# Kernel optimization log

Hardware: AMD Instinct MI355X
Metric: run time of the kernel (lower is better)

## Reference

```python
import jax, jax.numpy as jnp
import numpy as np

B, N, K, H = 8, 1024, 16, 4
EMB = 1024

def lrelu(x):
    return jnp.where(x >= 0, x, 0.2 * x)

def bn(x, g, b):
    # eval-mode BatchNorm with running_mean=0, running_var=1
    inv = 1.0 / np.sqrt(1.0 + 1e-5)
    shape = (1, -1) + (1,) * (x.ndim - 2)
    return x * (g * inv).reshape(shape) + b.reshape(shape)

def conv1x1(x, w):
    # 1x1 conv == channel matmul; x: (B,C,...), w: (O,C)
    return jnp.einsum('bc...,oc->bo...', x, w)

def knn_idx(x, k):
    # x: (B,C,N); negative squared pairwise distance, top-k largest = nearest
    inner = -2.0 * jnp.einsum('bcn,bcm->bnm', x, x)
    xx = jnp.sum(x * x, axis=1)                      # (B,N)
    pd = -xx[:, :, None] - inner - xx[:, None, :]
    return jax.lax.top_k(pd, k)[1]                   # (B,N,k)

def graph_feature(x, idx):
    b = x.shape[0]
    xt = jnp.transpose(x, (0, 2, 1))                 # (B,N,C)
    nbr = xt[jnp.arange(b)[:, None, None], idx]      # (B,N,K,C) gather
    ctr = jnp.broadcast_to(xt[:, :, None, :], nbr.shape)
    f = jnp.concatenate([nbr - ctr, ctr], axis=-1)   # (B,N,K,2C)
    return jnp.transpose(f, (0, 3, 1, 2))            # (B,2C,N,K)

def mak(x, y, w0, g0, b0, wm, gm, bm, w1, go, bo, ws, gs, bs, out_ch, in_ch):
    # Multi-head adaptive kernel: generate per-point (out,in,H) weights from y, apply to x
    Bc, _, Nc, Kc = x.shape
    y = lrelu(bn(conv1x1(y, w0), g0, b0))
    y = lrelu(bn(conv1x1(y, wm), gm, bm))
    y = conv1x1(y, w1)                               # (B, out*in*H, N, K)
    w = jnp.transpose(y, (0, 2, 3, 1)).reshape(Bc, Nc, Kc, out_ch, in_ch, H)
    xt = jnp.transpose(x, (0, 2, 3, 1))              # (B,N,K,in)
    # per-head matmul then sum over heads == single einsum over i and h
    out = jnp.einsum('bnkoih,bnki->bonk', w, xt)
    out = bn(out, go, bo)
    idt = bn(conv1x1(x, ws), gs, bs)                 # shortcut (in != out)
    return lrelu(out + idt)


def setup_inputs() -> dict:
    ks = jax.random.split(jax.random.key(0), 48)
    it = iter(range(48))
    def nrm(shape, fan):
        return jax.random.normal(ks[next(it)], shape, jnp.float32) / np.sqrt(fan)
    def gam(c):
        return jax.random.uniform(ks[next(it)], (c,), jnp.float32, 0.5, 1.5)
    def bet(c):
        return 0.1 * jax.random.normal(ks[next(it)], (c,), jnp.float32)
    d = {}
    d['x'] = jax.random.normal(ks[next(it)], (B, 3, N), jnp.float32)
    def mak_params(p, feat_c):
        d[p + '_w0'] = nrm((64, feat_c), feat_c); d[p + '_g0'] = gam(64); d[p + '_b0'] = bet(64)
        d[p + '_wm'] = nrm((64, 64), 64); d[p + '_gm'] = gam(64); d[p + '_bm'] = bet(64)
        d[p + '_w1'] = nrm((64 * 6 * H, 64), 64)
        d[p + '_go'] = gam(64); d[p + '_bo'] = bet(64)
        d[p + '_ws'] = nrm((64, 6), 6); d[p + '_gs'] = gam(64); d[p + '_bs'] = bet(64)
    mak_params('m1', 6)
    mak_params('m2', 128)
    d['w3'] = nrm((128, 128), 128); d['g3'] = gam(128); d['b3'] = bet(128)
    d['w4'] = nrm((256, 256), 256); d['g4'] = gam(256); d['b4'] = bet(256)
    d['w5'] = nrm((EMB, 512), 512); d['g5'] = gam(EMB); d['b5'] = bet(EMB)
    d['wl1'] = nrm((512, 2 * EMB), 2 * EMB); d['bn4_g'] = gam(512); d['bn4_b'] = bet(512)
    d['wl2'] = nrm((256, 512), 512); d['bl2'] = bet(256); d['bn5_g'] = gam(256); d['bn5_b'] = bet(256)
    d['wl3'] = nrm((49, 256), 256); d['bl3'] = bet(49)
    return d


def reference(x, m1_w0, m1_g0, m1_b0, m1_wm, m1_gm, m1_bm, m1_w1, m1_go, m1_bo, m1_ws, m1_gs, m1_bs, m2_w0, m2_g0, m2_b0, m2_wm, m2_gm, m2_bm, m2_w1, m2_go, m2_bo, m2_ws, m2_gs, m2_bs, w3, g3, b3, w4, g4, b4, w5, g5, b5, wl1, bn4_g, bn4_b, wl2, bl2, bn5_g, bn5_b, wl3, bl3):
    idx = knn_idx(x, K)                              # common_idx from points
    geo = graph_feature(x, idx)                      # (B,6,N,K); feat_x == geo_x at stage 1
    h = mak(geo, geo, m1_w0, m1_g0, m1_b0, m1_wm, m1_gm, m1_bm, m1_w1, m1_go, m1_bo, m1_ws, m1_gs, m1_bs, 64, 6)
    x1 = h.max(axis=-1)                              # (B,64,N)
    feat2 = graph_feature(x1, idx)                   # (B,128,N,K)
    h = mak(geo, feat2, m2_w0, m2_g0, m2_b0, m2_wm, m2_gm, m2_bm, m2_w1, m2_go, m2_bo, m2_ws, m2_gs, m2_bs, 64, 6)
    x2 = h.max(axis=-1)                              # (B,64,N)
    x3 = lrelu(bn(conv1x1(graph_feature(x2, idx), w3), g3, b3)).max(axis=-1)   # (B,128,N)
    x4 = lrelu(bn(conv1x1(graph_feature(x3, idx), w4), g4, b4)).max(axis=-1)   # (B,256,N)
    xc = jnp.concatenate([x1, x2, x3, x4], axis=1)   # (B,512,N)
    x5 = lrelu(bn(conv1x1(xc, w5), g5, b5))          # (B,EMB,N)
    xp = jnp.concatenate([x5.max(axis=-1), x5.mean(axis=-1)], axis=1)  # (B,2*EMB)
    xf = lrelu(bn(xp @ wl1.T, bn4_g, bn4_b))
    xf = lrelu(bn(xf @ wl2.T + bl2, bn5_g, bn5_b))
    return xf @ wl3.T + bl3                           # (B,49)
```

## Files before the change

### kernel.cpp

```cpp
#include <hip/hip_runtime.h>
#include <math.h>

#define BB 8
#define NN 1024
#define KK 16
#define NKP (NN*KK)
#define BN_INV 0.99999500003749981f

typedef unsigned short u16;
typedef __attribute__((ext_vector_type(8))) short short8;
typedef __attribute__((ext_vector_type(4))) float f32x4;

#define MFMA16(a,b,c) __builtin_amdgcn_mfma_f32_16x16x32_bf16(a,b,c,0,0,0)

__device__ __forceinline__ float lrelu(float v) { return v >= 0.f ? v : 0.2f * v; }

__device__ __forceinline__ u16 f2bf(float f) {
  union { float f; unsigned u; } v; v.f = f;
  unsigned r = v.u + 0x7fff + ((v.u >> 16) & 1);
  return (u16)(r >> 16);
}
__device__ __forceinline__ float bf2f(u16 s) {
  union { unsigned u; float f; } v; v.u = ((unsigned)s) << 16;
  return v.f;
}

constexpr size_t OFF_IDX   = 0;
constexpr size_t OFF_X1P   = 524288;
constexpr size_t OFF_X2P   = 1572864;
constexpr size_t OFF_X3P   = 2621440;
constexpr size_t OFF_X4P   = 4718592;
constexpr size_t OFF_PMAX  = 8912896;
constexpr size_t OFF_PSUM  = 9437184;
constexpr size_t OFF_XP    = 9961472;
constexpr size_t OFF_XF1   = 10027008;
constexpr size_t OFF_XF2   = 10043392;
constexpr size_t OFF_M1W0  = 10051584;
constexpr size_t OFF_M1WM  = 10055680;
constexpr size_t OFF_M1W1S = 10063872;
constexpr size_t OFF_M2W0  = 10117120;
constexpr size_t OFF_M2WM  = 10133504;
constexpr size_t OFF_M2W1S = 10141696;
constexpr size_t OFF_W3    = 10194944;
constexpr size_t OFF_W4    = 10227712;
constexpr size_t OFF_W5    = 10358784;
constexpr size_t OFF_WL1T  = 11407360;
constexpr size_t OFF_WL2T  = 15601664;
constexpr size_t OFF_WL3T  = 16125952;

struct SSeg { const float* w; const float* g; u16* dst; int O; int C; int cpl2; int ch; int start; };
struct SArgs { SSeg seg[7]; int total; };

__global__ __launch_bounds__(256) void prep_scale_bf16(SArgs a) {
  const int tid = blockIdx.x * 256 + threadIdx.x;
  if (tid >= a.total) return;
  int s = 0;
  #pragma unroll
  for (int i = 1; i < 7; ++i) if (tid >= a.seg[i].start) s = i;
  const SSeg sg = a.seg[s];
  const int e = tid - sg.start;
  const int o = e >> sg.cpl2;
  const int c = e & ((1 << sg.cpl2) - 1);
  float v = 0.f;
  if (c < sg.C) {
    v = sg.w[o * sg.C + c];
    if (sg.ch && c >= sg.ch) v -= sg.w[o * sg.C + c - sg.ch];
    v *= sg.g[o] * BN_INV;
  }
  sg.dst[(size_t)(c >> 5) * (sg.O * 32) + o * 32 + (c & 31)] = f2bf(v);
}

__global__ __launch_bounds__(256) void prep_w1s_bf16(
    const float* __restrict__ w1a, const float* __restrict__ wsa,
    const float* __restrict__ goa, const float* __restrict__ gsa,
    const float* __restrict__ w1b, const float* __restrict__ wsb,
    const float* __restrict__ gob, const float* __restrict__ gsb,
    u16* __restrict__ dsta, u16* __restrict__ dstb) {
  const int tid = blockIdx.x * 256 + threadIdx.x;
  if (tid >= 64 * 416) return;
  const float* w1 = blockIdx.y ? w1b : w1a;
  const float* wsm = blockIdx.y ? wsb : wsa;
  const float* go = blockIdx.y ? gob : goa;
  const float* gs = blockIdx.y ? gsb : gsa;
  u16* dst = blockIdx.y ? dstb : dsta;
  const int o = tid / 416, ci = tid - o * 416;
  float v = 0.f;
  if (ci < 384) {
    const int ii = ci >> 6, ch = ci & 63;
    const int base = (o * 24 + ii * 4) * 64 + ch;
    v = go[o] * BN_INV * (w1[base] + w1[base + 64] + w1[base + 128] + w1[base + 192]);
  } else if (ci < 390) {
    v = gs[o] * BN_INV * wsm[o * 6 + (ci - 384)];
  }
  dst[(size_t)(ci >> 5) * 2048 + o * 32 + (ci & 31)] = f2bf(v);
}

struct TSeg { const float* w; const float* g; float* dst; int O; int C; int start; };
struct TArgs3 { TSeg seg[3]; int total; };

__global__ __launch_bounds__(256) void prep_transpose_f32(TArgs3 a) {
  const int tid = blockIdx.x * 256 + threadIdx.x;
  if (tid >= a.total) return;
  int s = 0;
  #pragma unroll
  for (int i = 1; i < 3; ++i) if (tid >= a.seg[i].start) s = i;
  const TSeg sg = a.seg[s];
  const int e = tid - sg.start;
  const int c = e / sg.O;
  const int o = e - c * sg.O;
  float v = sg.w[o * sg.C + c];
  if (sg.g) v *= sg.g[o] * BN_INV;
  sg.dst[e] = v;
}

__global__ __launch_bounds__(256) void knn_kernel(const float* __restrict__ x, int* __restrict__ idxout) {
  const int wid  = (blockIdx.x * blockDim.x + threadIdx.x) >> 6;
  const int lane = threadIdx.x & 63;
  const int b = wid >> 10;
  const int n = wid & (NN - 1);
  const float* xb = x + b * 3 * NN;
  const float x0n = xb[n], x1n = xb[NN + n], x2n = xb[2 * NN + n];
  const float xxn = x0n * x0n + x1n * x1n + x2n * x2n;
  float pd[16];
  #pragma unroll
  for (int j = 0; j < 16; ++j) {
    const int m = j * 64 + lane;
    const float x0 = xb[m], x1 = xb[NN + m], x2 = xb[2 * NN + m];
    const float dot = x0n * x0 + x1n * x1 + x2n * x2;
    const float xxm = x0 * x0 + x1 * x1 + x2 * x2;
    pd[j] = 2.f * dot - xxn - xxm;
  }
  for (int r = 0; r < 16; ++r) {
    float bv = pd[0]; int bj = 0;
    #pragma unroll
    for (int j = 1; j < 16; ++j) if (pd[j] > bv) { bv = pd[j]; bj = j; }
    int bm = bj * 64 + lane;
    #pragma unroll
    for (int off = 32; off > 0; off >>= 1) {
      const float ov = __shfl_down(bv, off);
      const int   om = __shfl_down(bm, off);
      if (ov > bv || (ov == bv && om < bm)) { bv = ov; bm = om; }
    }
    bm = __shfl(bm, 0);
    if (lane == 0) idxout[wid * KK + r] = bm;
    const int  cj   = bm >> 6;
    const bool mine = (bm & 63) == lane;
    #pragma unroll
    for (int j = 0; j < 16; ++j) if (mine && j == cj) pd[j] = -INFINITY;
  }
}

__device__ __forceinline__ short8 bfrag64(const u16* T, int pl, int quad, int c0) {
  const int pos = ((c0 >> 3) + quad) ^ (pl & 7);
  return *(const short8*)(T + pl * 64 + pos * 8);
}
__device__ __forceinline__ void writeD64(u16* T, int pl, int quad, const f32x4 a,
                                         const float* __restrict__ bias, int obase) {
  union { ushort4 v; u16 s[4]; } pk;
  #pragma unroll
  for (int r = 0; r < 4; ++r) pk.s[r] = f2bf(lrelu(a[r] + bias[obase + quad * 4 + r]));
  const int g = (obase + quad * 4) >> 3;
  const int pos = g ^ (pl & 7);
  *(ushort4*)(T + pl * 64 + pos * 8 + (quad & 1) * 4) = pk.v;
}

template<int CIN_Y>
__global__ __launch_bounds__(256) void mak_mfma(
    const float* __restrict__ x, const int* __restrict__ idxb, const u16* __restrict__ srcp,
    const u16* __restrict__ w0b, const float* __restrict__ b0v,
    const u16* __restrict__ wmb, const float* __restrict__ bmv,
    const u16* __restrict__ w1s, const float* __restrict__ bov, const float* __restrict__ bsv,
    u16* __restrict__ Xoutp) {
  __shared__ __align__(16) u16 Y0s[64 * 64];
  __shared__ __align__(16) u16 YMs[64 * 64];
  __shared__ int nbrs[64];

  const int t = threadIdx.x;
  const int b = blockIdx.z;
  const int p0 = blockIdx.x * 64;
  const int w = t >> 6, l = t & 63;
  const int quad = l >> 4, l15 = l & 15;
  const int pl = w * 16 + l15;
  const int cq8 = quad * 8;
  const int nvtx = blockIdx.x * 4 + w;

  if (t < 64) nbrs[t] = idxb[b * NKP + p0 + t] & (NN - 1);
  __syncthreads();
  const int nbr = nbrs[pl];

  const float* xb = x + b * 3 * NN;
  float ge[6];
  #pragma unroll
  for (int i = 0; i < 3; ++i) {
    const float fc = xb[i * NN + nvtx];
    ge[i]     = xb[i * NN + nbr] - fc;
    ge[3 + i] = fc;
  }
  union { short8 v; u16 s[8]; } bg;
  bg.v = (short8)(short)0;
  if (quad == 0) {
    #pragma unroll
    for (int j = 0; j < 6; ++j) bg.s[j] = f2bf(ge[j]);
  }

  f32x4 acc[4];
  #pragma unroll
  for (int i = 0; i < 4; ++i) acc[i] = (f32x4)0.f;

  if constexpr (CIN_Y == 6) {
    #pragma unroll
    for (int at = 0; at < 4; ++at) {
      const short8 af = *(const short8*)(w0b + (size_t)(at * 16 + l15) * 32 + cq8);
      acc[at] = MFMA16(af, bg.v, acc[at]);
    }
  } else {
    short8 bf[4];
    #pragma unroll
    for (int k = 0; k < 2; ++k)
      bf[k] = *(const short8*)(srcp + (size_t)(b * NN + nbr) * 64 + k * 32 + cq8);
    #pragma unroll
    for (int k = 2; k < 4; ++k)
      bf[k] = *(const short8*)(srcp + (size_t)(b * NN + nvtx) * 64 + (k - 2) * 32 + cq8);
    #pragma unroll
    for (int k = 0; k < 4; ++k) {
      #pragma unroll
      for (int at = 0; at < 4; ++at) {
        const short8 af = *(const short8*)(w0b + (size_t)(k * 64 + at * 16 + l15) * 32 + cq8);
        acc[at] = MFMA16(af, bf[k], acc[at]);
      }
    }
  }
  #pragma unroll
  for (int at = 0; at < 4; ++at) writeD64(Y0s, pl, quad, acc[at], b0v, at * 16);
  __syncthreads();

  #pragma unroll
  for (int i = 0; i < 4; ++i) acc[i] = (f32x4)0.f;
  #pragma unroll
  for (int kc = 0; kc < 2; ++kc) {
    const short8 bf = bfrag64(Y0s, pl, quad, kc * 32);
    #pragma unroll
    for (int at = 0; at < 4; ++at) {
      const short8 af = *(const short8*)(wmb + (size_t)(kc * 64 + at * 16 + l15) * 32 + cq8);
      acc[at] = MFMA16(af, bf, acc[at]);
    }
  }
  #pragma unroll
  for (int at = 0; at < 4; ++at) writeD64(YMs, pl, quad, acc[at], bmv, at * 16);
  __syncthreads();

  #pragma unroll
  for (int i = 0; i < 4; ++i) acc[i] = (f32x4)0.f;
  #pragma unroll
  for (int ii = 0; ii < 6; ++ii) {
    f32x4 tacc[4];
    #pragma unroll
    for (int i = 0; i < 4; ++i) tacc[i] = (f32x4)0.f;
    #pragma unroll
    for (int kc = 0; kc < 2; ++kc) {
      const short8 bf = bfrag64(YMs, pl, quad, kc * 32);
      #pragma unroll
      for (int at = 0; at < 4; ++at) {
        const short8 af = *(const short8*)(w1s + (size_t)((ii * 2 + kc) * 64 + at * 16 + l15) * 32 + cq8);
        tacc[at] = MFMA16(af, bf, tacc[at]);
      }
    }
    const float g = ge[ii];
    #pragma unroll
    for (int at = 0; at < 4; ++at) acc[at] += g * tacc[at];
  }
  #pragma unroll
  for (int at = 0; at < 4; ++at) {
    const short8 af = *(const short8*)(w1s + (size_t)(12 * 64 + at * 16 + l15) * 32 + cq8);
    acc[at] = MFMA16(af, bg.v, acc[at]);
  }

  u16* orow = Xoutp + (size_t)(b * NN + nvtx) * 64;
  #pragma unroll
  for (int at = 0; at < 4; ++at) {
    union { ushort4 v; u16 s[4]; } pk;
    #pragma unroll
    for (int r = 0; r < 4; ++r) {
      const int o = at * 16 + quad * 4 + r;
      float v = lrelu(acc[at][r] + bov[o] + bsv[o]);
      v = fmaxf(v, __shfl_xor(v, 1));
      v = fmaxf(v, __shfl_xor(v, 2));
      v = fmaxf(v, __shfl_xor(v, 4));
      v = fmaxf(v, __shfl_xor(v, 8));
      pk.s[r] = f2bf(v);
    }
    if (l15 == 0) *(ushort4*)(orow + at * 16 + quad * 4) = pk.v;
  }
}

template<int CIN, int COUT>
__global__ __launch_bounds__(256) void conv_maxk_mfma(
    const u16* __restrict__ srcp, const int* __restrict__ idxb,
    const u16* __restrict__ wb, const float* __restrict__ bias,
    u16* __restrict__ Xoutp) {
  __shared__ int nbrs[64];
  constexpr int CH = CIN / 2;
  constexpr int NCH = CIN / 32;
  constexpr int NHB = CH / 32;
  constexpr int OPW = COUT / 4;
  constexpr int NAT = OPW / 16;

  const int t = threadIdx.x;
  const int b = blockIdx.z;
  const int p0 = blockIdx.x * 64;
  const int w = t >> 6, l = t & 63;
  const int quad = l >> 4, l15 = l & 15;
  const int cq8 = quad * 8;
  const int ow0 = w * OPW;

  if (t < 64) nbrs[t] = idxb[b * NKP + p0 + t] & (NN - 1);
  __syncthreads();

  int nbr[4], ctr[4];
  #pragma unroll
  for (int pg = 0; pg < 4; ++pg) {
    nbr[pg] = nbrs[pg * 16 + l15];
    ctr[pg] = blockIdx.x * 4 + pg;
  }

  f32x4 acc[NAT][4];
  #pragma unroll
  for (int i = 0; i < NAT; ++i)
    #pragma unroll
    for (int j = 0; j < 4; ++j) acc[i][j] = (f32x4)0.f;

  short8 bfr[NCH][4];
  #pragma unroll
  for (int k = 0; k < NHB; ++k) {
    const int c = k * 32 + cq8;
    #pragma unroll
    for (int pg = 0; pg < 4; ++pg)
      bfr[k][pg] = *(const short8*)(srcp + ((size_t)(b * NN + nbr[pg]) * CH + c));
  }
  #pragma unroll
  for (int k = NHB; k < NCH; ++k) {
    const int c = (k - NHB) * 32 + cq8;
    #pragma unroll
    for (int pg = 0; pg < 4; ++pg)
      bfr[k][pg] = *(const short8*)(srcp + ((size_t)(b * NN + ctr[pg]) * CH + c));
  }

  #pragma unroll
  for (int k = 0; k < NCH; ++k) {
    #pragma unroll
    for (int at = 0; at < NAT; ++at) {
      const short8 af = *(const short8*)(wb + ((size_t)(k * COUT + ow0 + at * 16 + l15)) * 32 + cq8);
      #pragma unroll
      for (int pg = 0; pg < 4; ++pg) acc[at][pg] = MFMA16(af, bfr[k][pg], acc[at][pg]);
    }
  }

  #pragma unroll
  for (int pg = 0; pg < 4; ++pg) {
    u16* orow = Xoutp + (size_t)(b * NN + ctr[pg]) * COUT + ow0;
    #pragma unroll
    for (int at = 0; at < NAT; ++at) {
      union { ushort4 v; u16 s[4]; } pk;
      #pragma unroll
      for (int r = 0; r < 4; ++r) {
        float v = lrelu(acc[at][pg][r] + bias[ow0 + at * 16 + quad * 4 + r]);
        v = fmaxf(v, __shfl_xor(v, 1));
        v = fmaxf(v, __shfl_xor(v, 2));
        v = fmaxf(v, __shfl_xor(v, 4));
        v = fmaxf(v, __shfl_xor(v, 8));
        pk.s[r] = f2bf(v);
      }
      if (l15 == 0) *(ushort4*)(orow + at * 16 + quad * 4) = pk.v;
    }
  }
}

__global__ __launch_bounds__(256) void conv5_mfma(
    const u16* __restrict__ X1P, const u16* __restrict__ X2P,
    const u16* __restrict__ X3P, const u16* __restrict__ X4P,
    const u16* __restrict__ w5b, const float* __restrict__ b5,
    float* __restrict__ PMAX, float* __restrict__ PSUM) {
  const int t = threadIdx.x;
  const int b = blockIdx.z;
  const int n0 = blockIdx.x * 64;
  const int w = t >> 6, l = t & 63;
  const int quad = l >> 4, l15 = l & 15;
  const int cq8 = quad * 8;
  const int ow0 = blockIdx.y * 256 + w * 64;

  f32x4 acc[4][4];
  #pragma unroll
  for (int i = 0; i < 4; ++i)
    #pragma unroll
    for (int j = 0; j < 4; ++j) acc[i][j] = (f32x4)0.f;

  #pragma unroll 4
  for (int k = 0; k < 16; ++k) {
    const int c = k * 32 + cq8;
    short8 bfr[4];
    #pragma unroll
    for (int pg = 0; pg < 4; ++pg) {
      const int n = n0 + pg * 16 + l15;
      const u16* src; int cc;
      if (c < 64)       { src = X1P + (size_t)(b * NN + n) * 64;  cc = c; }
      else if (c < 128) { src = X2P + (size_t)(b * NN + n) * 64;  cc = c - 64; }
      else if (c < 256) { src = X3P + (size_t)(b * NN + n) * 128; cc = c - 128; }
      else              { src = X4P + (size_t)(b * NN + n) * 256; cc = c - 256; }
      bfr[pg] = *(const short8*)(src + cc);
    }
    #pragma unroll
    for (int at = 0; at < 4; ++at) {
      const short8 af = *(const short8*)(w5b + ((size_t)(k * 1024 + ow0 + at * 16 + l15)) * 32 + cq8);
      #pragma unroll
      for (int pg = 0; pg < 4; ++pg) acc[at][pg] = MFMA16(af, bfr[pg], acc[at][pg]);
    }
  }

  #pragma unroll
  for (int at = 0; at < 4; ++at) {
    f32x4 pmx, psm;
    #pragma unroll
    for (int r = 0; r < 4; ++r) {
      const float bb = b5[ow0 + at * 16 + quad * 4 + r];
      float m = -INFINITY, s = 0.f;
      #pragma unroll
      for (int pg = 0; pg < 4; ++pg) {
        const float v = lrelu(acc[at][pg][r] + bb);
        m = fmaxf(m, v); s += v;
      }
      #pragma unroll
      for (int msk = 1; msk < 16; msk <<= 1) {
        m = fmaxf(m, __shfl_xor(m, msk));
        s += __shfl_xor(s, msk);
      }
      pmx[r] = m; psm[r] = s;
    }
    if (l15 == 0) {
      float* dm = PMAX + (size_t)(b * 16 + blockIdx.x) * 1024 + ow0 + at * 16 + quad * 4;
      float* ds = PSUM + (size_t)(b * 16 + blockIdx.x) * 1024 + ow0 + at * 16 + quad * 4;
      *(f32x4*)dm = pmx;
      *(f32x4*)ds = psm;
    }
  }
}

__global__ __launch_bounds__(256) void reduce5(const float* __restrict__ PMAX, const float* __restrict__ PSUM,
                                               float* __restrict__ XPg) {
  const int tid = blockIdx.x * 256 + threadIdx.x;
  const int b = tid >> 10, o = tid & 1023;
  float m = -INFINITY, s = 0.f;
  for (int pt = 0; pt < 16; ++pt) {
    m = fmaxf(m, PMAX[(size_t)(b * 16 + pt) * 1024 + o]);
    s += PSUM[(size_t)(b * 16 + pt) * 1024 + o];
  }
  XPg[b * 2048 + o] = m;
  XPg[b * 2048 + 1024 + o] = s * (1.f / 1024.f);
}

__global__ __launch_bounds__(256) void fc1_kernel(const float* __restrict__ XPg, const float* __restrict__ wl1t,
                                                  const float* __restrict__ bn4_b, float* __restrict__ XF1) {
  __shared__ float red[64 * 5];
  const int t = threadIdx.x;
  const int b = blockIdx.y;
  const int o = blockIdx.x * 64 + (t & 63);
  const int cq = t >> 6;
  const float* xp = XPg + b * 2048;
  float acc = 0.f;
  for (int c = cq * 512; c < cq * 512 + 512; ++c) acc = fmaf(wl1t[c * 512 + o], xp[c], acc);
  red[(t & 63) * 5 + cq] = acc;
  __syncthreads();
  if (t < 64) {
    const int oo = blockIdx.x * 64 + t;
    const float v = red[t * 5] + red[t * 5 + 1] + red[t * 5 + 2] + red[t * 5 + 3] + bn4_b[oo];
    XF1[b * 512 + oo] = lrelu(v);
  }
}

__global__ __launch_bounds__(256) void fc2_kernel(const float* __restrict__ XF1, const float* __restrict__ wl2t,
                                                  const float* __restrict__ bl2, const float* __restrict__ bn5_g,
                                                  const float* __restrict__ bn5_b, float* __restrict__ XF2) {
  __shared__ float red[64 * 5];
  const int t = threadIdx.x;
  const int b = blockIdx.y;
  const int o = blockIdx.x * 64 + (t & 63);
  const int cq = t >> 6;
  const float* xf = XF1 + b * 512;
  float acc = 0.f;
  for (int c = cq * 128; c < cq * 128 + 128; ++c) acc = fmaf(wl2t[c * 256 + o], xf[c], acc);
  red[(t & 63) * 5 + cq] = acc;
  __syncthreads();
  if (t < 64) {
    const int oo = blockIdx.x * 64 + t;
    const float bias = bl2[oo] * (bn5_g[oo] * BN_INV) + bn5_b[oo];
    const float v = red[t * 5] + red[t * 5 + 1] + red[t * 5 + 2] + red[t * 5 + 3] + bias;
    XF2[b * 256 + oo] = lrelu(v);
  }
}

__global__ __launch_bounds__(256) void fc3_kernel(const float* __restrict__ XF2, const float* __restrict__ wl3t,
                                                  const float* __restrict__ bl3, float* __restrict__ out) {
  __shared__ float red[64 * 5];
  const int t = threadIdx.x;
  const int b = blockIdx.y;
  const int ol = t & 63;
  const int cq = t >> 6;
  const float* xf = XF2 + b * 256;
  float acc = 0.f;
  if (ol < 49) for (int c = cq * 64; c < cq * 64 + 64; ++c) acc = fmaf(wl3t[c * 49 + ol], xf[c], acc);
  red[ol * 5 + cq] = acc;
  __syncthreads();
  if (t < 49) out[b * 49 + t] = red[t * 5] + red[t * 5 + 1] + red[t * 5 + 2] + red[t * 5 + 3] + bl3[t];
}

extern "C" void kernel_launch(void* const* d_in, const int* in_sizes, int n_in,
                              void* d_out, int out_size, void* d_ws, size_t ws_size,
                              hipStream_t stream) {
  (void)in_sizes; (void)n_in; (void)out_size; (void)ws_size;
  const float* x     = (const float*)d_in[0];
  const float* m1_w0 = (const float*)d_in[1];
  const float* m1_g0 = (const float*)d_in[2];
  const float* m1_b0 = (const float*)d_in[3];
  const float* m1_wm = (const float*)d_in[4];
  const float* m1_gm = (const float*)d_in[5];
  const float* m1_bm = (const float*)d_in[6];
  const float* m1_w1 = (const float*)d_in[7];
  const float* m1_go = (const float*)d_in[8];
  const float* m1_bo = (const float*)d_in[9];
  const float* m1_ws = (const float*)d_in[10];
  const float* m1_gs = (const float*)d_in[11];
  const float* m1_bs = (const float*)d_in[12];
  const float* m2_w0 = (const float*)d_in[13];
  const float* m2_g0 = (const float*)d_in[14];
  const float* m2_b0 = (const float*)d_in[15];
  const float* m2_wm = (const float*)d_in[16];
  const float* m2_gm = (const float*)d_in[17];
  const float* m2_bm = (const float*)d_in[18];
  const float* m2_w1 = (const float*)d_in[19];
  const float* m2_go = (const float*)d_in[20];
  const float* m2_bo = (const float*)d_in[21];
  const float* m2_ws = (const float*)d_in[22];
  const float* m2_gs = (const float*)d_in[23];
  const float* m2_bs = (const float*)d_in[24];
  const float* w3    = (const float*)d_in[25];
  const float* g3    = (const float*)d_in[26];
  const float* b3    = (const float*)d_in[27];
  const float* w4    = (const float*)d_in[28];
  const float* g4    = (const float*)d_in[29];
  const float* b4    = (const float*)d_in[30];
  const float* w5    = (const float*)d_in[31];
  const float* g5    = (const float*)d_in[32];
  const float* b5    = (const float*)d_in[33];
  const float* wl1   = (const float*)d_in[34];
  const float* bn4_g = (const float*)d_in[35];
  const float* bn4_b = (const float*)d_in[36];
  const float* wl2   = (const float*)d_in[37];
  const float* bl2   = (const float*)d_in[38];
  const float* bn5_g = (const float*)d_in[39];
  const float* bn5_b = (const float*)d_in[40];
  const float* wl3   = (const float*)d_in[41];
  const float* bl3   = (const float*)d_in[42];

  char* wsb = (char*)d_ws;
  int*  IDX  = (int*)(wsb + OFF_IDX);
  u16*  X1P  = (u16*)(wsb + OFF_X1P);
  u16*  X2P  = (u16*)(wsb + OFF_X2P);
  u16*  X3P  = (u16*)(wsb + OFF_X3P);
  u16*  X4P  = (u16*)(wsb + OFF_X4P);
  float* PMAX = (float*)(wsb + OFF_PMAX);
  float* PSUM = (float*)(wsb + OFF_PSUM);
  float* XPg  = (float*)(wsb + OFF_XP);
  float* XF1  = (float*)(wsb + OFF_XF1);
  float* XF2  = (float*)(wsb + OFF_XF2);
  u16*  M1W0 = (u16*)(wsb + OFF_M1W0);
  u16*  M1WM = (u16*)(wsb + OFF_M1WM);
  u16*  M1W1S = (u16*)(wsb + OFF_M1W1S);
  u16*  M2W0 = (u16*)(wsb + OFF_M2W0);
  u16*  M2WM = (u16*)(wsb + OFF_M2WM);
  u16*  M2W1S = (u16*)(wsb + OFF_M2W1S);
  u16*  W3B  = (u16*)(wsb + OFF_W3);
  u16*  W4B  = (u16*)(wsb + OFF_W4);
  u16*  W5B  = (u16*)(wsb + OFF_W5);
  float* WL1T = (float*)(wsb + OFF_WL1T);
  float* WL2T = (float*)(wsb + OFF_WL2T);
  float* WL3T = (float*)(wsb + OFF_WL3T);

  SArgs sa; int st = 0;
  auto sset = [&](int i, const float* w, const float* g, u16* dst, int O, int C, int cpl2, int ch) {
    sa.seg[i].w = w; sa.seg[i].g = g; sa.seg[i].dst = dst; sa.seg[i].O = O; sa.seg[i].C = C;
    sa.seg[i].cpl2 = cpl2; sa.seg[i].ch = ch; sa.seg[i].start = st; st += O << cpl2;
  };
  sset(0, m1_w0, m1_g0, M1W0, 64, 6, 5, 0);
  sset(1, m1_wm, m1_gm, M1WM, 64, 64, 6, 0);
  sset(2, m2_w0, m2_g0, M2W0, 64, 128, 7, 64);
  sset(3, m2_wm, m2_gm, M2WM, 64, 64, 6, 0);
  sset(4, w3, g3, W3B, 128, 128, 7, 64);
  sset(5, w4, g4, W4B, 256, 256, 8, 128);
  sset(6, w5, g5, W5B, 1024, 512, 9, 0);
  sa.total = st;

  TArgs3 ta; int tt = 0;
  auto tset = [&](int i, const float* w, const float* g, float* dst, int O, int C) {
    ta.seg[i].w = w; ta.seg[i].g = g; ta.seg[i].dst = dst; ta.seg[i].O = O; ta.seg[i].C = C;
    ta.seg[i].start = tt; tt += O * C;
  };
  tset(0, wl1, bn4_g, WL1T, 512, 2048);
  tset(1, wl2, bn5_g, WL2T, 256, 512);
  tset(2, wl3, nullptr, WL3T, 49, 256);
  ta.total = tt;

  hipLaunchKernelGGL(prep_scale_bf16, dim3((sa.total + 255) / 256), dim3(256), 0, stream, sa);
  hipLaunchKernelGGL(prep_w1s_bf16, dim3(104, 2), dim3(256), 0, stream,
                     m1_w1, m1_ws, m1_go, m1_gs, m2_w1, m2_ws, m2_go, m2_gs, M1W1S, M2W1S);
  hipLaunchKernelGGL(prep_transpose_f32, dim3((ta.total + 255) / 256), dim3(256), 0, stream, ta);

  hipLaunchKernelGGL(knn_kernel, dim3(2048), dim3(256), 0, stream, x, IDX);

  hipLaunchKernelGGL((mak_mfma<6>), dim3(256, 1, BB), dim3(256), 0, stream,
                     x, IDX, (const u16*)nullptr, M1W0, m1_b0, M1WM, m1_bm, M1W1S, m1_bo, m1_bs, X1P);
  hipLaunchKernelGGL((mak_mfma<128>), dim3(256, 1, BB), dim3(256), 0, stream,
                     x, IDX, X1P, M2W0, m2_b0, M2WM, m2_bm, M2W1S, m2_bo, m2_bs, X2P);

  hipLaunchKernelGGL((conv_maxk_mfma<128, 128>), dim3(256, 1, BB), dim3(256), 0, stream,
                     X2P, IDX, W3B, b3, X3P);
  hipLaunchKernelGGL((conv_maxk_mfma<256, 256>), dim3(256, 1, BB), dim3(256), 0, stream,
                     X3P, IDX, W4B, b4, X4P);

  hipLaunchKernelGGL(conv5_mfma, dim3(16, 4, BB), dim3(256), 0, stream,
                     X1P, X2P, X3P, X4P, W5B, b5, PMAX, PSUM);
  hipLaunchKernelGGL(reduce5, dim3(32), dim3(256), 0, stream, PMAX, PSUM, XPg);

  hipLaunchKernelGGL(fc1_kernel, dim3(8, BB), dim3(256), 0, stream, XPg, WL1T, bn4_b, XF1);
  hipLaunchKernelGGL(fc2_kernel, dim3(4, BB), dim3(256), 0, stream, XF1, WL2T, bl2, bn5_g, bn5_b, XF2);
  hipLaunchKernelGGL(fc3_kernel, dim3(1, BB), dim3(256), 0, stream, XF2, WL3T, bl3, (float*)d_out);
}
```

Before: 435.2 us.

## Assign one point per wave with all output channels in conv_maxk_mfma

Restructures the neighbor-conv kernel so that each wave handles one point's 16 neighbors across all output channels, where before each wave handled a quarter of the channels for four points. This removes the shared-memory neighbor index staging and the block-wide barrier, and each wave loads its own gather rows directly. In exchange, every wave now loads the full weight matrix instead of a quarter of it, so weight traffic per block goes up by four times. Accumulator registers per lane stay about the same, since NAT grows while the per-point dimension is dropped.

```diff
diff --git a/kernel.cpp b/kernel.cpp
--- a/kernel.cpp
+++ b/kernel.cpp
@@ -298,80 +298,57 @@
     const u16* __restrict__ srcp, const int* __restrict__ idxb,
     const u16* __restrict__ wb, const float* __restrict__ bias,
     u16* __restrict__ Xoutp) {
-  __shared__ int nbrs[64];
   constexpr int CH = CIN / 2;
   constexpr int NCH = CIN / 32;
   constexpr int NHB = CH / 32;
-  constexpr int OPW = COUT / 4;
-  constexpr int NAT = OPW / 16;
+  constexpr int NAT = COUT / 16;
 
   const int t = threadIdx.x;
   const int b = blockIdx.z;
-  const int p0 = blockIdx.x * 64;
   const int w = t >> 6, l = t & 63;
   const int quad = l >> 4, l15 = l & 15;
   const int cq8 = quad * 8;
-  const int ow0 = w * OPW;
-
-  if (t < 64) nbrs[t] = idxb[b * NKP + p0 + t] & (NN - 1);
-  __syncthreads();
-
-  int nbr[4], ctr[4];
-  #pragma unroll
-  for (int pg = 0; pg < 4; ++pg) {
-    nbr[pg] = nbrs[pg * 16 + l15];
-    ctr[pg] = blockIdx.x * 4 + pg;
-  }
-
-  f32x4 acc[NAT][4];
-  #pragma unroll
-  for (int i = 0; i < NAT; ++i)
-    #pragma unroll
-    for (int j = 0; j < 4; ++j) acc[i][j] = (f32x4)0.f;
-
-  short8 bfr[NCH][4];
-  #pragma unroll
-  for (int k = 0; k < NHB; ++k) {
-    const int c = k * 32 + cq8;
-    #pragma unroll
-    for (int pg = 0; pg < 4; ++pg)
-      bfr[k][pg] = *(const short8*)(srcp + ((size_t)(b * NN + nbr[pg]) * CH + c));
-  }
-  #pragma unroll
-  for (int k = NHB; k < NCH; ++k) {
-    const int c = (k - NHB) * 32 + cq8;
-    #pragma unroll
-    for (int pg = 0; pg < 4; ++pg)
-      bfr[k][pg] = *(const short8*)(srcp + ((size_t)(b * NN + ctr[pg]) * CH + c));
-  }
+  const int pt = blockIdx.x * 4 + w;
+
+  const int nbr = idxb[b * NKP + pt * 16 + l15] & (NN - 1);
+
+  f32x4 acc[NAT];
+  #pragma unroll
+  for (int i = 0; i < NAT; ++i) acc[i] = (f32x4)0.f;
+
+  short8 bfr[NCH];
+  const u16* nrow = srcp + (size_t)(b * NN + nbr) * CH;
+  const u16* crow = srcp + (size_t)(b * NN + pt) * CH;
+  #pragma unroll
+  for (int k = 0; k < NHB; ++k)
+    bfr[k] = *(const short8*)(nrow + k * 32 + cq8);
+  #pragma unroll
+  for (int k = NHB; k < NCH; ++k)
+    bfr[k] = *(const short8*)(crow + (k - NHB) * 32 + cq8);
 
   #pragma unroll
   for (int k = 0; k < NCH; ++k) {
     #pragma unroll
     for (int at = 0; at < NAT; ++at) {
-      const short8 af = *(const short8*)(wb + ((size_t)(k * COUT + ow0 + at * 16 + l15)) * 32 + cq8);
-      #pragma unroll
-      for (int pg = 0; pg < 4; ++pg) acc[at][pg] = MFMA16(af, bfr[k][pg], acc[at][pg]);
-    }
-  }
-
-  #pragma unroll
-  for (int pg = 0; pg < 4; ++pg) {
-    u16* orow = Xoutp + (size_t)(b * NN + ctr[pg]) * COUT + ow0;
-    #pragma unroll
-    for (int at = 0; at < NAT; ++at) {
-      union { ushort4 v; u16 s[4]; } pk;
-      #pragma unroll
-      for (int r = 0; r < 4; ++r) {
-        float v = lrelu(acc[at][pg][r] + bias[ow0 + at * 16 + quad * 4 + r]);
-        v = fmaxf(v, __shfl_xor(v, 1));
-        v = fmaxf(v, __shfl_xor(v, 2));
-        v = fmaxf(v, __shfl_xor(v, 4));
-        v = fmaxf(v, __shfl_xor(v, 8));
-        pk.s[r] = f2bf(v);
-      }
-      if (l15 == 0) *(ushort4*)(orow + at * 16 + quad * 4) = pk.v;
-    }
+      const short8 af = *(const short8*)(wb + ((size_t)(k * COUT + at * 16 + l15)) * 32 + cq8);
+      acc[at] = MFMA16(af, bfr[k], acc[at]);
+    }
+  }
+
+  u16* orow = Xoutp + (size_t)(b * NN + pt) * COUT;
+  #pragma unroll
+  for (int at = 0; at < NAT; ++at) {
+    union { ushort4 v; u16 s[4]; } pk;
+    #pragma unroll
+    for (int r = 0; r < 4; ++r) {
+      float v = lrelu(acc[at][r] + bias[at * 16 + quad * 4 + r]);
+      v = fmaxf(v, __shfl_xor(v, 1));
+      v = fmaxf(v, __shfl_xor(v, 2));
+      v = fmaxf(v, __shfl_xor(v, 4));
+      v = fmaxf(v, __shfl_xor(v, 8));
+      pk.s[r] = f2bf(v);
+    }
+    if (l15 == 0) *(ushort4*)(orow + at * 16 + quad * 4) = pk.v;
   }
 }
 
```

Result: slower. 477.1 us (+9.6%).

## Factor edge convs into per-point dense GEMM plus gather-max

Applied to the files above, without the earlier changes.

Conv3 and conv4 on edge features are split algebraically: W·[x_j - x_i, x_i] = W_a·x_j + (W_b - W_a)·x_i. Both terms are computed once per point with a stacked dense MFMA GEMM into a UV buffer. A separate gather kernel then adds the neighbor U and center V terms, applies leaky ReLU and takes the max over K. This removes the K-fold redundant matmul work per point, at the cost of an extra kernel launch, an intermediate bf16 buffer round-trip and rounding of the partial sums to bf16.

```diff
diff --git a/kernel.cpp b/kernel.cpp
--- a/kernel.cpp
+++ b/kernel.cpp
@@ -41,14 +41,16 @@
 constexpr size_t OFF_M2W0  = 10117120;
 constexpr size_t OFF_M2WM  = 10133504;
 constexpr size_t OFF_M2W1S = 10141696;
-constexpr size_t OFF_W3    = 10194944;
-constexpr size_t OFF_W4    = 10227712;
+constexpr size_t OFF_W3S   = 10194944;
+constexpr size_t OFF_W4S   = 10227712;
 constexpr size_t OFF_W5    = 10358784;
 constexpr size_t OFF_WL1T  = 11407360;
 constexpr size_t OFF_WL2T  = 15601664;
 constexpr size_t OFF_WL3T  = 16125952;
-
-struct SSeg { const float* w; const float* g; u16* dst; int O; int C; int cpl2; int ch; int start; };
+constexpr size_t OFF_UV3   = 16177152;
+constexpr size_t OFF_UV4   = 20371456;
+
+struct SSeg { const float* w; const float* g; u16* dst; int O; int C; int cpl2; int ch; int stk; int start; };
 struct SArgs { SSeg seg[7]; int total; };
 
 __global__ __launch_bounds__(256) void prep_scale_bf16(SArgs a) {
@@ -59,15 +61,22 @@
   for (int i = 1; i < 7; ++i) if (tid >= a.seg[i].start) s = i;
   const SSeg sg = a.seg[s];
   const int e = tid - sg.start;
-  const int o = e >> sg.cpl2;
+  const int o2 = e >> sg.cpl2;
   const int c = e & ((1 << sg.cpl2) - 1);
   float v = 0.f;
-  if (c < sg.C) {
-    v = sg.w[o * sg.C + c];
-    if (sg.ch && c >= sg.ch) v -= sg.w[o * sg.C + c - sg.ch];
+  if (sg.stk) {
+    const int half = sg.O >> 1;
+    const int o = o2 & (half - 1);
+    const int CIN = 2 * sg.C;
+    const float wd = sg.w[o * CIN + c];
+    v = (o2 < half) ? wd : (sg.w[o * CIN + sg.C + c] - wd);
     v *= sg.g[o] * BN_INV;
-  }
-  sg.dst[(size_t)(c >> 5) * (sg.O * 32) + o * 32 + (c & 31)] = f2bf(v);
+  } else if (c < sg.C) {
+    v = sg.w[o2 * sg.C + c];
+    if (sg.ch && c >= sg.ch) v -= sg.w[o2 * sg.C + c - sg.ch];
+    v *= sg.g[o2] * BN_INV;
+  }
+  sg.dst[(size_t)(c >> 5) * (sg.O * 32) + o2 * 32 + (c & 31)] = f2bf(v);
 }
 
 __global__ __launch_bounds__(256) void prep_w1s_bf16(
@@ -293,86 +302,102 @@
   }
 }
 
-template<int CIN, int COUT>
-__global__ __launch_bounds__(256) void conv_maxk_mfma(
-    const u16* __restrict__ srcp, const int* __restrict__ idxb,
-    const u16* __restrict__ wb, const float* __restrict__ bias,
-    u16* __restrict__ Xoutp) {
-  __shared__ int nbrs[64];
-  constexpr int CH = CIN / 2;
-  constexpr int NCH = CIN / 32;
-  constexpr int NHB = CH / 32;
-  constexpr int OPW = COUT / 4;
-  constexpr int NAT = OPW / 16;
-
+template<int CH, int COUT2>
+__global__ __launch_bounds__(256) void dense_uv(
+    const u16* __restrict__ srcp, const u16* __restrict__ w2,
+    const float* __restrict__ bias, u16* __restrict__ UV) {
+  constexpr int COUT = COUT2 / 2;
+  constexpr int NCH = CH / 32;
   const int t = threadIdx.x;
   const int b = blockIdx.z;
-  const int p0 = blockIdx.x * 64;
+  const int n0 = blockIdx.x * 64;
   const int w = t >> 6, l = t & 63;
   const int quad = l >> 4, l15 = l & 15;
   const int cq8 = quad * 8;
-  const int ow0 = w * OPW;
-
-  if (t < 64) nbrs[t] = idxb[b * NKP + p0 + t] & (NN - 1);
-  __syncthreads();
-
-  int nbr[4], ctr[4];
-  #pragma unroll
-  for (int pg = 0; pg < 4; ++pg) {
-    nbr[pg] = nbrs[pg * 16 + l15];
-    ctr[pg] = blockIdx.x * 4 + pg;
-  }
-
-  f32x4 acc[NAT][4];
-  #pragma unroll
-  for (int i = 0; i < NAT; ++i)
+  const int ow0 = blockIdx.y * 256 + w * 64;
+
+  f32x4 acc[4][4];
+  #pragma unroll
+  for (int i = 0; i < 4; ++i)
     #pragma unroll
     for (int j = 0; j < 4; ++j) acc[i][j] = (f32x4)0.f;
 
-  short8 bfr[NCH][4];
-  #pragma unroll
-  for (int k = 0; k < NHB; ++k) {
-    const int c = k * 32 + cq8;
-    #pragma unroll
-    for (int pg = 0; pg < 4; ++pg)
-      bfr[k][pg] = *(const short8*)(srcp + ((size_t)(b * NN + nbr[pg]) * CH + c));
-  }
-  #pragma unroll
-  for (int k = NHB; k < NCH; ++k) {
-    const int c = (k - NHB) * 32 + cq8;
-    #pragma unroll
-    for (int pg = 0; pg < 4; ++pg)
-      bfr[k][pg] = *(const short8*)(srcp + ((size_t)(b * NN + ctr[pg]) * CH + c));
-  }
-
   #pragma unroll
   for (int k = 0; k < NCH; ++k) {
-    #pragma unroll
-    for (int at = 0; at < NAT; ++at) {
-      const short8 af = *(const short8*)(wb + ((size_t)(k * COUT + ow0 + at * 16 + l15)) * 32 + cq8);
+    short8 bfr[4];
+    #pragma unroll
+    for (int pg = 0; pg < 4; ++pg) {
+      const int n = n0 + pg * 16 + l15;
+      bfr[pg] = *(const short8*)(srcp + (size_t)(b * NN + n) * CH + k * 32 + cq8);
+    }
+    #pragma unroll
+    for (int at = 0; at < 4; ++at) {
+      const short8 af = *(const short8*)(w2 + ((size_t)(k * COUT2 + ow0 + at * 16 + l15)) * 32 + cq8);
       #pragma unroll
-      for (int pg = 0; pg < 4; ++pg) acc[at][pg] = MFMA16(af, bfr[k][pg], acc[at][pg]);
-    }
-  }
-
-  #pragma unroll
-  for (int pg = 0; pg < 4; ++pg) {
-    u16* orow = Xoutp + (size_t)(b * NN + ctr[pg]) * COUT + ow0;
-    #pragma unroll
-    for (int at = 0; at < NAT; ++at) {
+      for (int pg = 0; pg < 4; ++pg) acc[at][pg] = MFMA16(af, bfr[pg], acc[at][pg]);
+    }
+  }
+
+  #pragma unroll
+  for (int at = 0; at < 4; ++at) {
+    const int o0 = ow0 + at * 16 + quad * 4;
+    const bool isv = (o0 >= COUT);
+    float bb[4];
+    #pragma unroll
+    for (int r = 0; r < 4; ++r) bb[r] = isv ? bias[o0 + r - COUT] : 0.f;
+    #pragma unroll
+    for (int pg = 0; pg < 4; ++pg) {
+      const int n = n0 + pg * 16 + l15;
       union { ushort4 v; u16 s[4]; } pk;
       #pragma unroll
-      for (int r = 0; r < 4; ++r) {
-        float v = lrelu(acc[at][pg][r] + bias[ow0 + at * 16 + quad * 4 + r]);
-        v = fmaxf(v, __shfl_xor(v, 1));
-        v = fmaxf(v, __shfl_xor(v, 2));
-        v = fmaxf(v, __shfl_xor(v, 4));
-        v = fmaxf(v, __shfl_xor(v, 8));
-        pk.s[r] = f2bf(v);
-      }
-      if (l15 == 0) *(ushort4*)(orow + at * 16 + quad * 4) = pk.v;
-    }
-  }
+      for (int r = 0; r < 4; ++r) pk.s[r] = f2bf(acc[at][pg][r] + bb[r]);
+      *(ushort4*)(UV + (size_t)(b * NN + n) * COUT2 + o0) = pk.v;
+    }
+  }
+}
+
+__device__ __forceinline__ float4 ubf4(ushort4 q) {
+  float4 f;
+  f.x = bf2f(q.x); f.y = bf2f(q.y); f.z = bf2f(q.z); f.w = bf2f(q.w);
+  return f;
+}
+
+template<int COUT>
+__global__ __launch_bounds__(256) void gather_max(
+    const u16* __restrict__ UV, const int* __restrict__ idxb,
+    u16* __restrict__ Xoutp) {
+  constexpr int CG = COUT / 4;
+  const int tid = blockIdx.x * 256 + threadIdx.x;
+  const int cg = tid & (CG - 1);
+  const int P = tid / CG;
+  const int b = P >> 10;
+  const int n = P & (NN - 1);
+
+  const float4 vv = ubf4(*(const ushort4*)(UV + (size_t)P * (2 * COUT) + COUT + 4 * cg));
+  const int4* ip = (const int4*)(idxb + (size_t)b * NKP + n * 16);
+  float4 m = {-INFINITY, -INFINITY, -INFINITY, -INFINITY};
+  #pragma unroll
+  for (int kq = 0; kq < 4; ++kq) {
+    const int4 iv = ip[kq];
+    const int mr[4] = { iv.x & (NN - 1), iv.y & (NN - 1), iv.z & (NN - 1), iv.w & (NN - 1) };
+    ushort4 uq[4];
+    #pragma unroll
+    for (int j = 0; j < 4; ++j)
+      uq[j] = *(const ushort4*)(UV + (size_t)(b * NN + mr[j]) * (2 * COUT) + 4 * cg);
+    #pragma unroll
+    for (int j = 0; j < 4; ++j) {
+      const float4 uu = ubf4(uq[j]);
+      float4 s;
+      s.x = uu.x + vv.x; s.y = uu.y + vv.y; s.z = uu.z + vv.z; s.w = uu.w + vv.w;
+      m.x = fmaxf(m.x, fmaxf(s.x, 0.2f * s.x));
+      m.y = fmaxf(m.y, fmaxf(s.y, 0.2f * s.y));
+      m.z = fmaxf(m.z, fmaxf(s.z, 0.2f * s.z));
+      m.w = fmaxf(m.w, fmaxf(s.w, 0.2f * s.w));
+    }
+  }
+  union { ushort4 v; u16 s[4]; } pk;
+  pk.s[0] = f2bf(m.x); pk.s[1] = f2bf(m.y); pk.s[2] = f2bf(m.z); pk.s[3] = f2bf(m.w);
+  *(ushort4*)(Xoutp + (size_t)P * COUT + 4 * cg) = pk.v;
 }
 
 __global__ __launch_bounds__(256) void conv5_mfma(
@@ -577,25 +602,28 @@
   u16*  M2W0 = (u16*)(wsb + OFF_M2W0);
   u16*  M2WM = (u16*)(wsb + OFF_M2WM);
   u16*  M2W1S = (u16*)(wsb + OFF_M2W1S);
-  u16*  W3B  = (u16*)(wsb + OFF_W3);
-  u16*  W4B  = (u16*)(wsb + OFF_W4);
+  u16*  W3S  = (u16*)(wsb + OFF_W3S);
+  u16*  W4S  = (u16*)(wsb + OFF_W4S);
   u16*  W5B  = (u16*)(wsb + OFF_W5);
   float* WL1T = (float*)(wsb + OFF_WL1T);
   float* WL2T = (float*)(wsb + OFF_WL2T);
   float* WL3T = (float*)(wsb + OFF_WL3T);
+  u16*  UV3  = (u16*)(wsb + OFF_UV3);
+  u16*  UV4  = (u16*)(wsb + OFF_UV4);
 
   SArgs sa; int st = 0;
-  auto sset = [&](int i, const float* w, const float* g, u16* dst, int O, int C, int cpl2, int ch) {
+  auto sset = [&](int i, const float* w, const float* g, u16* dst, int O, int C, int cpl2, int ch, int stk) {
     sa.seg[i].w = w; sa.seg[i].g = g; sa.seg[i].dst = dst; sa.seg[i].O = O; sa.seg[i].C = C;
-    sa.seg[i].cpl2 = cpl2; sa.seg[i].ch = ch; sa.seg[i].start = st; st += O << cpl2;
+    sa.seg[i].cpl2 = cpl2; sa.seg[i].ch = ch; sa.seg[i].stk = stk; sa.seg[i].start = st;
+    st += O << cpl2;
   };
-  sset(0, m1_w0, m1_g0, M1W0, 64, 6, 5, 0);
-  sset(1, m1_wm, m1_gm, M1WM, 64, 64, 6, 0);
-  sset(2, m2_w0, m2_g0, M2W0, 64, 128, 7, 64);
-  sset(3, m2_wm, m2_gm, M2WM, 64, 64, 6, 0);
-  sset(4, w3, g3, W3B, 128, 128, 7, 64);
-  sset(5, w4, g4, W4B, 256, 256, 8, 128);
-  sset(6, w5, g5, W5B, 1024, 512, 9, 0);
+  sset(0, m1_w0, m1_g0, M1W0, 64, 6, 5, 0, 0);
+  sset(1, m1_wm, m1_gm, M1WM, 64, 64, 6, 0, 0);
+  sset(2, m2_w0, m2_g0, M2W0, 64, 128, 7, 64, 0);
+  sset(3, m2_wm, m2_gm, M2WM, 64, 64, 6, 0, 0);
+  sset(4, w3, g3, W3S, 256, 64, 6, 0, 1);
+  sset(5, w4, g4, W4S, 512, 128, 7, 0, 1);
+  sset(6, w5, g5, W5B, 1024, 512, 9, 0, 0);
   sa.total = st;
 
   TArgs3 ta; int tt = 0;
@@ -620,10 +648,11 @@
   hipLaunchKernelGGL((mak_mfma<128>), dim3(256, 1, BB), dim3(256), 0, stream,
                      x, IDX, X1P, M2W0, m2_b0, M2WM, m2_bm, M2W1S, m2_bo, m2_bs, X2P);
 
-  hipLaunchKernelGGL((conv_maxk_mfma<128, 128>), dim3(256, 1, BB), dim3(256), 0, stream,
-                     X2P, IDX, W3B, b3, X3P);
-  hipLaunchKernelGGL((conv_maxk_mfma<256, 256>), dim3(256, 1, BB), dim3(256), 0, stream,
-                     X3P, IDX, W4B, b4, X4P);
+  hipLaunchKernelGGL((dense_uv<64, 256>), dim3(16, 1, BB), dim3(256), 0, stream, X2P, W3S, b3, UV3);
+  hipLaunchKernelGGL((gather_max<128>), dim3(1024), dim3(256), 0, stream, UV3, IDX, X3P);
+
+  hipLaunchKernelGGL((dense_uv<128, 512>), dim3(16, 2, BB), dim3(256), 0, stream, X3P, W4S, b4, UV4);
+  hipLaunchKernelGGL((gather_max<256>), dim3(2048), dim3(256), 0, stream, UV4, IDX, X4P);
 
   hipLaunchKernelGGL(conv5_mfma, dim3(16, 4, BB), dim3(256), 0, stream,
                      X1P, X2P, X3P, X4P, W5B, b5, PMAX, PSUM);
```

Result: faster. 389.5 us (-10.5%).
